# Performance work log

Measured on AMD Instinct MI355X. Metric: run time of the kernel, lower is better.

The kernel has to match this reference:

```python
import jax, jax.numpy as jnp
import numpy as np

D_MODEL = 1024
NUM_HEADS = 16
D_K = D_MODEL // NUM_HEADS
B, S = 2, 2048
LN_EPS = 1e-5


def setup_inputs() -> dict:
    key = jax.random.key(0)
    ks = jax.random.split(key, 11)
    sc = 1.0 / np.sqrt(D_MODEL)
    return {
        "x": jax.random.normal(ks[0], (B, S, D_MODEL), dtype=jnp.float32),
        "Wq": jax.random.normal(ks[1], (D_MODEL, D_MODEL), dtype=jnp.float32) * sc,
        "bq": jnp.zeros((D_MODEL,), dtype=jnp.float32),
        "Wk": jax.random.normal(ks[2], (D_MODEL, D_MODEL), dtype=jnp.float32) * sc,
        "bk": jnp.zeros((D_MODEL,), dtype=jnp.float32),
        "Wv": jax.random.normal(ks[3], (D_MODEL, D_MODEL), dtype=jnp.float32) * sc,
        "bv": jnp.zeros((D_MODEL,), dtype=jnp.float32),
        "Wo": jax.random.normal(ks[4], (D_MODEL, D_MODEL), dtype=jnp.float32) * sc,
        "bo": jnp.zeros((D_MODEL,), dtype=jnp.float32),
        "ln_gamma": jnp.ones((D_MODEL,), dtype=jnp.float32),
        "ln_beta": jnp.zeros((D_MODEL,), dtype=jnp.float32),
    }


def reference(x, Wq, bq, Wk, bk, Wv, bv, Wo, bo, ln_gamma, ln_beta):
    b, s, d = x.shape
    # QKV projections -> [B, H, S, D_K]
    def split_heads(y):
        return y.reshape(b, s, NUM_HEADS, D_K).transpose(0, 2, 1, 3)
    q = split_heads(x @ Wq + bq)
    k = split_heads(x @ Wk + bk)
    v = split_heads(x @ Wv + bv)
    # scores [B, H, S, S]; dropout is identity in eval mode
    scores = jnp.einsum("bhqd,bhkd->bhqk", q, k) / jnp.sqrt(jnp.float32(D_K))
    attn = jax.nn.softmax(scores, axis=-1)
    context = jnp.einsum("bhqk,bhkd->bhqd", attn, v)
    context = context.transpose(0, 2, 1, 3).reshape(b, s, d)
    out = context @ Wo + bo
    # residual + LayerNorm (eps=1e-5, torch default)
    h = x + out
    mu = jnp.mean(h, axis=-1, keepdims=True)
    var = jnp.var(h, axis=-1, keepdims=True)
    return (h - mu) / jnp.sqrt(var + LN_EPS) * ln_gamma + ln_beta
```

## Files before the change

### kernel.cpp

```cpp
#include <hip/hip_runtime.h>
#include <math.h>

#define D_MODEL 1024
#define NHEAD   16
#define DKK     64
#define BATCH   2
#define SEQ     2048
#define MROWS   (BATCH*SEQ)

typedef __attribute__((ext_vector_type(8)))  short bf16x8;
typedef __attribute__((ext_vector_type(4)))  short bf16x4;
typedef __attribute__((ext_vector_type(4)))  float f32x4;
typedef __attribute__((ext_vector_type(16))) float f32x16;

#define MFMA(a,b,c)   __builtin_amdgcn_mfma_f32_16x16x32_bf16((a),(b),(c),0,0,0)
#define MFMA32(a,b,c) __builtin_amdgcn_mfma_f32_32x32x16_bf16((a),(b),(c),0,0,0)

#define QSCALE 0.18033688f

#define SBAR() { __builtin_amdgcn_sched_barrier(0); \
                 __builtin_amdgcn_s_barrier();      \
                 __builtin_amdgcn_sched_barrier(0); }

#define CH  520
#define TIL (8*CH)

__device__ __forceinline__ short f2b(float f) {
    unsigned u = __float_as_uint(f);
    unsigned r = (u + 0x7FFFu + ((u >> 16) & 1u)) >> 16;
    return (short)r;
}

__device__ __forceinline__ float fexp2(float x) {
    float r; asm("v_exp_f32 %0, %1" : "=v"(r) : "v"(x)); return r;
}

__device__ __forceinline__ void gld_lds16(const void* g, void* l) {
    __builtin_amdgcn_global_load_lds(
        (const __attribute__((address_space(1))) void*)g,
        (__attribute__((address_space(3))) void*)l, 16, 0, 0);
}

__global__ __launch_bounds__(256)
void prep_weights(const float* __restrict__ Wq, const float* __restrict__ Wk,
                  const float* __restrict__ Wv, const float* __restrict__ Wo,
                  short* __restrict__ wt3, short* __restrict__ wot)
{
    const int z = blockIdx.z;
    const float* W = z==0 ? Wq : z==1 ? Wk : z==2 ? Wv : Wo;
    short* dst = (z < 3) ? (wt3 + (size_t)z*1024*1024) : wot;
    __shared__ float tile[32][33];
    const int tx = threadIdx.x & 31, ty = threadIdx.x >> 5;
    const int c0 = blockIdx.x*32, r0 = blockIdx.y*32;
    #pragma unroll
    for (int i = 0; i < 4; i++)
        tile[ty + i*8][tx] = W[(size_t)(r0 + ty + i*8)*1024 + c0 + tx];
    __syncthreads();
    #pragma unroll
    for (int i = 0; i < 4; i++)
        dst[(size_t)(c0 + ty + i*8)*1024 + r0 + tx] = f2b(tile[tx][ty + i*8]);
}

__global__ __launch_bounds__(256)
void convert_x(const float* __restrict__ x, short* __restrict__ xb)
{
    const int i = (blockIdx.x*256 + threadIdx.x) * 8;
    float4 a = *(const float4*)(x + i);
    float4 c = *(const float4*)(x + i + 4);
    bf16x8 v;
    v[0]=f2b(a.x); v[1]=f2b(a.y); v[2]=f2b(a.z); v[3]=f2b(a.w);
    v[4]=f2b(c.x); v[5]=f2b(c.y); v[6]=f2b(c.z); v[7]=f2b(c.w);
    *(bf16x8*)(xb + i) = v;
}

__global__ __launch_bounds__(512, 2)
void gemm_qkv(const short* __restrict__ A, const short* __restrict__ Bt,
              const float* __restrict__ bq, const float* __restrict__ bk,
              const float* __restrict__ bv,
              short* __restrict__ qb, short* __restrict__ kb, short* __restrict__ vtb)
{
    __shared__ short Ab[2*16384];
    __shared__ short Bb[2*12288];

    const int t = threadIdx.x;
    const int w = t >> 6, lane = t & 63;
    const int r = lane & 15, g4 = lane >> 4;
    const int wm = w >> 2, wn = w & 3;

    const int bid = blockIdx.x;
    const int xcd = bid & 7, idx = bid >> 3;
    const int mi  = (xcd >> 1) * 4 + (idx & 3);
    const int ni  = (xcd & 1) * 8 + (idx >> 2);
    const int m0 = mi * 256, n0 = ni * 192;

    const int srow = t >> 3;
    const int scol = ((t & 7) ^ (srow & 7)) * 8;

    f32x4 acc[8][3] = {};
    bf16x8 bfr[2][3];

#define QKV_STAGE(P, KT)                                                      \
    { const int kk = (KT) * 64 + scol;                                        \
      _Pragma("unroll")                                                       \
      for (int a = 0; a < 4; a++)                                             \
          gld_lds16(A + (size_t)(m0 + a*64 + srow)*1024 + kk,                 \
                    Ab + (P)*16384 + a*4096 + t*8);                           \
      _Pragma("unroll")                                                       \
      for (int p2 = 0; p2 < 3; p2++)                                          \
          gld_lds16(Bt + (size_t)(n0 + p2*64 + srow)*1024 + kk,               \
                    Bb + (P)*12288 + p2*4096 + t*8); }

#define QKV_PHASE(P, MH, KS, LOADB)                                           \
    { const short* Abase = Ab + (P)*16384 + wm*8192;                          \
      bf16x8 af[4];                                                           \
      _Pragma("unroll")                                                       \
      for (int i = 0; i < 4; i++)                                             \
          af[i] = *(const bf16x8*)&Abase[((MH)*64 + i*16 + r)*64 +            \
                                         (((KS)*4 + g4) ^ (r&7))*8];          \
      if (LOADB) {                                                            \
          const short* Bbase = Bb + (P)*12288;                                \
          _Pragma("unroll")                                                   \
          for (int j = 0; j < 3; j++)                                         \
              bfr[KS][j] = *(const bf16x8*)&Bbase[(wn*48 + j*16 + r)*64 +     \
                                                  (((KS)*4 + g4) ^ (r&7))*8]; \
      }                                                                       \
      SBAR();                                                                 \
      __builtin_amdgcn_s_setprio(1);                                          \
      _Pragma("unroll")                                                       \
      for (int i = 0; i < 4; i++)                                             \
          _Pragma("unroll")                                                   \
          for (int j = 0; j < 3; j++)                                         \
              acc[(MH)*4+i][j] = MFMA(af[i], bfr[KS][j], acc[(MH)*4+i][j]);   \
      __builtin_amdgcn_s_setprio(0);                                          \
      SBAR(); }

    QKV_STAGE(0, 0)
    QKV_STAGE(1, 1)
    asm volatile("s_waitcnt vmcnt(7)" ::: "memory");
    __builtin_amdgcn_s_barrier();
    __builtin_amdgcn_sched_barrier(0);

    int p = 0;
    #pragma unroll 1
    for (int kt = 0; kt < 16; kt++) {
        QKV_PHASE(p, 0, 0, 1)
        QKV_PHASE(p, 1, 0, 0)
        QKV_PHASE(p, 0, 1, 1)
        QKV_PHASE(p, 1, 1, 0)
        if (kt < 14) {
            QKV_STAGE(p, kt + 2)
            asm volatile("s_waitcnt vmcnt(7)" ::: "memory");
        } else {
            asm volatile("s_waitcnt vmcnt(0)" ::: "memory");
        }
        __builtin_amdgcn_s_barrier();
        __builtin_amdgcn_sched_barrier(0);
        p ^= 1;
    }
#undef QKV_STAGE
#undef QKV_PHASE

    #pragma unroll
    for (int n = 0; n < 3; n++) {
        const int colbase = n0 + wn*48 + n*16;
        const int proj    = colbase >> 10;
        const int within  = colbase & 1023;
        const int h       = within >> 6;
        const int d       = (within & 63) + r;
        const float* bias = (proj == 0) ? bq : (proj == 1) ? bk : bv;
        const float bval  = bias[within + r];
        #pragma unroll
        for (int m = 0; m < 8; m++) {
            const int growb = m0 + wm*128 + m*16 + g4*4;
            const int bidx  = growb >> 11;
            const int s     = growb & 2047;
            if (proj == 0) {
                #pragma unroll
                for (int i = 0; i < 4; i++)
                    qb[((size_t)(bidx*NHEAD + h)*SEQ + s + i)*DKK + d] =
                        f2b((acc[m][n][i] + bval) * QSCALE);
            } else if (proj == 1) {
                #pragma unroll
                for (int i = 0; i < 4; i++)
                    kb[((size_t)(bidx*NHEAD + h)*SEQ + s + i)*DKK + d] =
                        f2b(acc[m][n][i] + bval);
            } else {
                bf16x4 pk;
                #pragma unroll
                for (int i = 0; i < 4; i++) pk[i] = f2b(acc[m][n][i] + bval);
                *(bf16x4*)(vtb + ((size_t)(bidx*NHEAD + h)*DKK + d)*SEQ + s) = pk;
            }
        }
    }
}

__global__ __launch_bounds__(256)
void gemm_out(const short* __restrict__ A, const short* __restrict__ Bt,
              const float* __restrict__ bo, const float* __restrict__ resid,
              float* __restrict__ hb)
{
    __shared__ short As[2*128*32];
    __shared__ short Bs[2*64*32];
    const int t = threadIdx.x;
    const int w = t >> 6, lane = t & 63;
    const int r = lane & 15, g4 = lane >> 4;
    const int wr = w >> 1, wc = w & 1;

    const int bid = blockIdx.x;
    const int xcd = bid & 7, idx = bid >> 3;
    const int mi  = (xcd >> 1) * 8 + (idx & 7);
    const int ni  = (xcd & 1) * 8 + (idx >> 3);
    const int m0 = mi * 128, n0 = ni * 64;

    const int srow = lane >> 2, su = lane & 3;

    f32x4 acc[4][2] = {};

#define OUT_STAGE(BUF, K0)                                                     \
    { const int kk = (K0) & 1023;                                              \
      _Pragma("unroll")                                                        \
      for (int c = 0; c < 2; c++) {                                            \
          const int row = w*32 + c*16 + srow;                                  \
          gld_lds16(A + (size_t)(m0+row)*1024 + kk + 8*(su ^ ((row>>1)&3)),    \
                    As + (BUF)*4096 + w*1024 + c*512);                         \
      }                                                                        \
      { const int row = w*16 + srow;                                           \
        gld_lds16(Bt + (size_t)(n0+row)*1024 + kk + 8*(su ^ ((row>>1)&3)),     \
                  Bs + (BUF)*2048 + w*512); } }

    OUT_STAGE(0, 0)
    __syncthreads();

    int cur = 0;
    #pragma unroll 1
    for (int k0 = 0; k0 < 1024; k0 += 32) {
        OUT_STAGE(cur^1, k0 + 32)
        const short* Abase = As + cur*4096;
        const short* Bbase = Bs + cur*2048;
        bf16x8 af[4], bfr[2];
        #pragma unroll
        for (int m = 0; m < 4; m++) {
            const int row = wr*64 + m*16 + r;
            af[m] = *(const bf16x8*)&Abase[row*32 + (g4 ^ ((row>>1)&3))*8];
        }
        #pragma unroll
        for (int n = 0; n < 2; n++) {
            const int row = wc*32 + n*16 + r;
            bfr[n] = *(const bf16x8*)&Bbase[row*32 + (g4 ^ ((row>>1)&3))*8];
        }
        __builtin_amdgcn_s_setprio(1);
        #pragma unroll
        for (int m = 0; m < 4; m++)
            #pragma unroll
            for (int n = 0; n < 2; n++)
                acc[m][n] = MFMA(af[m], bfr[n], acc[m][n]);
        __builtin_amdgcn_s_setprio(0);
        __syncthreads();
        cur ^= 1;
    }
#undef OUT_STAGE

    #pragma unroll
    for (int n = 0; n < 2; n++) {
        const int col = n0 + wc*32 + n*16 + r;
        const float bval = bo[col];
        #pragma unroll
        for (int m = 0; m < 4; m++) {
            #pragma unroll
            for (int i = 0; i < 4; i++) {
                const int grow = m0 + wr*64 + m*16 + g4*4 + i;
                const size_t ofs = (size_t)grow*1024 + col;
                hb[ofs] = acc[m][n][i] + bval + resid[ofs];
            }
        }
    }
}

__global__ __launch_bounds__(256, 3)
void attn_mfma(const short* __restrict__ Q, const short* __restrict__ K,
               const short* __restrict__ VT, short* __restrict__ ctx)
{
    __shared__ short Ks[2*TIL];
    __shared__ short Vs[2*TIL];

    const int t = threadIdx.x;
    const int w = t >> 6, lane = t & 63;
    const int l31 = lane & 31, hi = lane >> 5;
    const int srow8 = lane >> 3, su = lane & 7;
    const int lane8 = lane * 8;
    const int swz8  = (su ^ srow8) * 8;

    const int bid     = blockIdx.x;
    const int logical = (bid & 7) * 64 + (bid >> 3);
    const int bh_lin  = logical >> 4;
    const int qt      = logical & 15;
    const int b = bh_lin >> 4, h = bh_lin & 15;
    const int q0 = qt * 128 + w * 32;

    const size_t bh = (size_t)b * NHEAD + h;
    const short* Qp = Q  + bh * SEQ * DKK;
    const short* Kp = K  + bh * SEQ * DKK;
    const short* Vp = VT + bh * DKK * SEQ;

    const short* kstage = Kp + (size_t)(w*8 + srow8) * DKK + swz8;
    const short* vstage = Vp + (size_t)(w*8 + srow8) * SEQ + swz8;

    bf16x8 qf[4];
    #pragma unroll
    for (int d0 = 0; d0 < 4; d0++)
        qf[d0] = *(const bf16x8*)(Qp + (size_t)(q0 + l31)*DKK + d0*16 + hi*8);

    int koff[8], voff[8];
    #pragma unroll
    for (int i = 0; i < 8; i++) {
        const int kchunk = (i>>2)*4 + (l31>>3);
        koff[i] = kchunk*CH + (l31&7)*64 + ((((i&3)*2 + hi) ^ (l31&7)) * 8);
        const int vchunk = (i&1)*4 + (l31>>3);
        voff[i] = vchunk*CH + (l31&7)*64 + ((((i>>1)*2 + hi) ^ (l31&7)) * 8);
    }

    f32x16 o0 = {}, o1 = {};
    float lrow = 0.f;

#define ATT_STAGE(KDST, VDST, J)                                               \
    { const size_t jj = (size_t)((J) & (SEQ-1));                               \
      const short* ksrc = kstage + jj*DKK;                                     \
      gld_lds16(ksrc,           (KDST) + w*CH + lane8);                        \
      gld_lds16(ksrc + 32*DKK,  (KDST) + (4+w)*CH + lane8);                    \
      const short* vsrc = vstage + jj;                                         \
      gld_lds16(vsrc,           (VDST) + w*CH + lane8);                        \
      gld_lds16(vsrc + 32*SEQ,  (VDST) + (4+w)*CH + lane8); }

    ATT_STAGE(Ks, Vs, 0)
    __syncthreads();

    int cur = 0;
    #pragma unroll 1
    for (int j0 = 0; j0 < SEQ; j0 += 64) {
        ATT_STAGE(Ks + (cur^1)*TIL, Vs + (cur^1)*TIL, j0 + 64)

        const short* Kb = Ks + cur*TIL;
        const short* Vb = Vs + cur*TIL;

        bf16x8 kf[8];
        #pragma unroll
        for (int i = 0; i < 8; i++) kf[i] = *(const bf16x8*)&Kb[koff[i]];
        f32x16 s0 = {}, s1 = {};
        __builtin_amdgcn_s_setprio(1);
        #pragma unroll
        for (int d0 = 0; d0 < 4; d0++) s0 = MFMA32(kf[d0],   qf[d0], s0);
        #pragma unroll
        for (int d0 = 0; d0 < 4; d0++) s1 = MFMA32(kf[4+d0], qf[d0], s1);
        __builtin_amdgcn_s_setprio(0);

        #pragma unroll
        for (int r = 0; r < 16; r++) s0[r] = fexp2(s0[r]);
        #pragma unroll
        for (int r = 0; r < 16; r++) s1[r] = fexp2(s1[r]);
        float ts[16];
        #pragma unroll
        for (int r = 0; r < 16; r++) ts[r] = s0[r] + s1[r];
        #pragma unroll
        for (int dd = 8; dd >= 1; dd >>= 1)
            #pragma unroll
            for (int r = 0; r < dd; r++) ts[r] += ts[r + dd];
        lrow += ts[0] + __shfl_xor(ts[0], 32);

        bf16x8 vf[8];
        #pragma unroll
        for (int i = 0; i < 8; i++) vf[i] = *(const bf16x8*)&Vb[voff[i]];

        #pragma unroll
        for (int ks = 0; ks < 4; ks++) {
            const int g = (ks & 1) * 8;
            float e0,e1,e2,e3,e4,e5,e6,e7;
            if (ks < 2) { e0=s0[g+0];e1=s0[g+1];e2=s0[g+2];e3=s0[g+3];
                          e4=s0[g+4];e5=s0[g+5];e6=s0[g+6];e7=s0[g+7]; }
            else        { e0=s1[g+0];e1=s1[g+1];e2=s1[g+2];e3=s1[g+3];
                          e4=s1[g+4];e5=s1[g+5];e6=s1[g+6];e7=s1[g+7]; }
            unsigned u0,u1,u2,u3;
            asm("v_cvt_pk_bf16_f32 %0, %1, %2" : "=v"(u0) : "v"(e0), "v"(e1));
            asm("v_cvt_pk_bf16_f32 %0, %1, %2" : "=v"(u1) : "v"(e2), "v"(e3));
            asm("v_cvt_pk_bf16_f32 %0, %1, %2" : "=v"(u2) : "v"(e4), "v"(e5));
            asm("v_cvt_pk_bf16_f32 %0, %1, %2" : "=v"(u3) : "v"(e6), "v"(e7));
            auto rA = __builtin_amdgcn_permlane32_swap(u0, u2, false, false);
            auto rB = __builtin_amdgcn_permlane32_swap(u1, u3, false, false);
            union { unsigned u[4]; bf16x8 v; } pa;
            pa.u[0] = rA[0]; pa.u[1] = rB[0]; pa.u[2] = rA[1]; pa.u[3] = rB[1];
            __builtin_amdgcn_s_setprio(1);
            o0 = MFMA32(pa.v, vf[ks*2+0], o0);
            o1 = MFMA32(pa.v, vf[ks*2+1], o1);
            __builtin_amdgcn_s_setprio(0);
        }

        __syncthreads();
        cur ^= 1;
    }

    const float li = 1.f / lrow;
    const int lb = __float_as_int(li);
    #pragma unroll
    for (int r = 0; r < 16; r++) {
        const int crow = (r&3) + 8*(r>>2) + 4*hi;
        const float lv = __int_as_float(__builtin_amdgcn_ds_bpermute(crow*4, lb));
        const size_t base = ((size_t)b*SEQ + q0 + crow)*D_MODEL + h*DKK + l31;
        ctx[base]      = f2b(o0[r] * lv);
        ctx[base + 32] = f2b(o1[r] * lv);
    }
#undef ATT_STAGE
}

__global__ __launch_bounds__(256)
void ln_kernel(const float* __restrict__ hbuf, const float* __restrict__ gamma,
               const float* __restrict__ beta, float* __restrict__ out)
{
    const int row = blockIdx.x;
    const int t = threadIdx.x;
    const float* hp = hbuf + (size_t)row * D_MODEL;
    float4 v = ((const float4*)hp)[t];
    float sum = v.x + v.y + v.z + v.w;
    float sq  = v.x*v.x + v.y*v.y + v.z*v.z + v.w*v.w;
    #pragma unroll
    for (int o = 1; o <= 32; o <<= 1) {
        sum += __shfl_xor(sum, o);
        sq  += __shfl_xor(sq, o);
    }
    __shared__ float s1[4], s2[4];
    if ((t & 63) == 0) { s1[t >> 6] = sum; s2[t >> 6] = sq; }
    __syncthreads();
    sum = s1[0] + s1[1] + s1[2] + s1[3];
    sq  = s2[0] + s2[1] + s2[2] + s2[3];
    const float mean = sum * (1.0f / D_MODEL);
    const float var  = sq * (1.0f / D_MODEL) - mean * mean;
    const float inv  = rsqrtf(var + 1e-5f);
    float4 g  = ((const float4*)gamma)[t];
    float4 be = ((const float4*)beta)[t];
    float4 rr;
    rr.x = (v.x - mean) * inv * g.x + be.x;
    rr.y = (v.y - mean) * inv * g.y + be.y;
    rr.z = (v.z - mean) * inv * g.z + be.z;
    rr.w = (v.w - mean) * inv * g.w + be.w;
    ((float4*)(out + (size_t)row * D_MODEL))[t] = rr;
}

extern "C" void kernel_launch(void* const* d_in, const int* in_sizes, int n_in,
                              void* d_out, int out_size, void* d_ws, size_t ws_size,
                              hipStream_t stream)
{
    const float* x  = (const float*)d_in[0];
    const float* Wq = (const float*)d_in[1];
    const float* bq = (const float*)d_in[2];
    const float* Wk = (const float*)d_in[3];
    const float* bk = (const float*)d_in[4];
    const float* Wv = (const float*)d_in[5];
    const float* bv = (const float*)d_in[6];
    const float* Wo = (const float*)d_in[7];
    const float* bo = (const float*)d_in[8];
    const float* g  = (const float*)d_in[9];
    const float* be = (const float*)d_in[10];

    short* xb  = (short*)d_ws;
    short* wt3 = xb  + (size_t)4096*1024;
    short* wot = wt3 + (size_t)3072*1024;
    short* qb  = wot + (size_t)1024*1024;
    short* kb  = qb  + (size_t)4096*1024;
    short* vtb = kb  + (size_t)4096*1024;
    short* cxb = vtb + (size_t)4096*1024;
    float* hb  = (float*)(cxb + (size_t)4096*1024);

    prep_weights<<<dim3(32,32,4), 256, 0, stream>>>(Wq, Wk, Wv, Wo, wt3, wot);
    convert_x  <<<2048, 256, 0, stream>>>(x, xb);
    gemm_qkv   <<<256, 512, 0, stream>>>(xb, wt3, bq, bk, bv, qb, kb, vtb);
    attn_mfma  <<<512, 256, 0, stream>>>(qb, kb, vtb, cxb);
    gemm_out   <<<512, 256, 0, stream>>>(cxb, wot, bo, x, hb);
    ln_kernel  <<<MROWS, 256, 0, stream>>>(hb, g, be, (float*)d_out);
}
```

Before: 124.7 us.

## Process two KV tiles per attention iteration with split accumulators

The attention loop now stages and processes 128 keys per iteration as two 64-key sub-tiles, with double-buffered LDS holding four tiles. The two halves use independent score and output accumulators, summed at the end. The aim is to halve the barrier count and give the scheduler more independent MFMA chains to overlap. In exchange LDS and register use roughly double, so launch bounds drop from 3 to 2 blocks per SIMD, lowering occupancy.

```diff
diff --git a/kernel.cpp b/kernel.cpp
--- a/kernel.cpp
+++ b/kernel.cpp
@@ -276,12 +276,12 @@
     }
 }
 
-__global__ __launch_bounds__(256, 3)
+__global__ __launch_bounds__(256, 2)
 void attn_mfma(const short* __restrict__ Q, const short* __restrict__ K,
                const short* __restrict__ VT, short* __restrict__ ctx)
 {
-    __shared__ short Ks[2*TIL];
-    __shared__ short Vs[2*TIL];
+    __shared__ short Ks[4*TIL];
+    __shared__ short Vs[4*TIL];
 
     const int t = threadIdx.x;
     const int w = t >> 6, lane = t & 63;
@@ -319,7 +319,7 @@
         voff[i] = vchunk*CH + (l31&7)*64 + ((((i>>1)*2 + hi) ^ (l31&7)) * 8);
     }
 
-    f32x16 o0 = {}, o1 = {};
+    f32x16 o0A = {}, o1A = {}, o0B = {}, o1B = {};
     float lrow = 0.f;
 
 #define ATT_STAGE(KDST, VDST, J)                                               \
@@ -331,67 +331,82 @@
       gld_lds16(vsrc,           (VDST) + w*CH + lane8);                        \
       gld_lds16(vsrc + 32*SEQ,  (VDST) + (4+w)*CH + lane8); }
 
-    ATT_STAGE(Ks, Vs, 0)
+#define QK_SUB(KB, S0, S1)                                                     \
+    { bf16x8 kf[8];                                                            \
+      _Pragma("unroll")                                                        \
+      for (int i = 0; i < 8; i++) kf[i] = *(const bf16x8*)&(KB)[koff[i]];      \
+      _Pragma("unroll")                                                        \
+      for (int d0 = 0; d0 < 4; d0++) S0 = MFMA32(kf[d0],   qf[d0], S0);        \
+      _Pragma("unroll")                                                        \
+      for (int d0 = 0; d0 < 4; d0++) S1 = MFMA32(kf[4+d0], qf[d0], S1); }
+
+#define PV_SUB(S0, S1, VB, O0, O1)                                             \
+    { bf16x8 vf[8];                                                            \
+      _Pragma("unroll")                                                        \
+      for (int i = 0; i < 8; i++) vf[i] = *(const bf16x8*)&(VB)[voff[i]];      \
+      _Pragma("unroll")                                                        \
+      for (int ks = 0; ks < 4; ks++) {                                         \
+        const int g = (ks & 1) * 8;                                            \
+        float e0,e1,e2,e3,e4,e5,e6,e7;                                         \
+        if (ks < 2) { e0=S0[g+0];e1=S0[g+1];e2=S0[g+2];e3=S0[g+3];             \
+                      e4=S0[g+4];e5=S0[g+5];e6=S0[g+6];e7=S0[g+7]; }           \
+        else        { e0=S1[g+0];e1=S1[g+1];e2=S1[g+2];e3=S1[g+3];             \
+                      e4=S1[g+4];e5=S1[g+5];e6=S1[g+6];e7=S1[g+7]; }           \
+        unsigned u0,u1,u2,u3;                                                  \
+        asm("v_cvt_pk_bf16_f32 %0, %1, %2" : "=v"(u0) : "v"(e0), "v"(e1));     \
+        asm("v_cvt_pk_bf16_f32 %0, %1, %2" : "=v"(u1) : "v"(e2), "v"(e3));     \
+        asm("v_cvt_pk_bf16_f32 %0, %1, %2" : "=v"(u2) : "v"(e4), "v"(e5));     \
+        asm("v_cvt_pk_bf16_f32 %0, %1, %2" : "=v"(u3) : "v"(e6), "v"(e7));     \
+        auto rA = __builtin_amdgcn_permlane32_swap(u0, u2, false, false);      \
+        auto rB = __builtin_amdgcn_permlane32_swap(u1, u3, false, false);      \
+        union { unsigned u[4]; bf16x8 v; } pa;                                 \
+        pa.u[0] = rA[0]; pa.u[1] = rB[0]; pa.u[2] = rA[1]; pa.u[3] = rB[1];    \
+        O0 = MFMA32(pa.v, vf[ks*2+0], O0);                                     \
+        O1 = MFMA32(pa.v, vf[ks*2+1], O1);                                     \
+      } }
+
+    ATT_STAGE(Ks,       Vs,       0)
+    ATT_STAGE(Ks + TIL, Vs + TIL, 64)
     __syncthreads();
 
     int cur = 0;
     #pragma unroll 1
-    for (int j0 = 0; j0 < SEQ; j0 += 64) {
-        ATT_STAGE(Ks + (cur^1)*TIL, Vs + (cur^1)*TIL, j0 + 64)
-
-        const short* Kb = Ks + cur*TIL;
-        const short* Vb = Vs + cur*TIL;
-
-        bf16x8 kf[8];
-        #pragma unroll
-        for (int i = 0; i < 8; i++) kf[i] = *(const bf16x8*)&Kb[koff[i]];
-        f32x16 s0 = {}, s1 = {};
-        __builtin_amdgcn_s_setprio(1);
-        #pragma unroll
-        for (int d0 = 0; d0 < 4; d0++) s0 = MFMA32(kf[d0],   qf[d0], s0);
-        #pragma unroll
-        for (int d0 = 0; d0 < 4; d0++) s1 = MFMA32(kf[4+d0], qf[d0], s1);
-        __builtin_amdgcn_s_setprio(0);
-
-        #pragma unroll
-        for (int r = 0; r < 16; r++) s0[r] = fexp2(s0[r]);
-        #pragma unroll
-        for (int r = 0; r < 16; r++) s1[r] = fexp2(s1[r]);
+    for (int j0 = 0; j0 < SEQ; j0 += 128) {
+        {
+            const int nb = (cur^1)*2*TIL;
+            ATT_STAGE(Ks + nb,       Vs + nb,       j0 + 128)
+            ATT_STAGE(Ks + nb + TIL, Vs + nb + TIL, j0 + 192)
+        }
+
+        const short* KbA = Ks + cur*2*TIL;
+        const short* VbA = Vs + cur*2*TIL;
+        const short* KbB = KbA + TIL;
+        const short* VbB = VbA + TIL;
+
+        f32x16 s0A = {}, s1A = {}, s0B = {}, s1B = {};
+        QK_SUB(KbA, s0A, s1A)
+        QK_SUB(KbB, s0B, s1B)
+
+        #pragma unroll
+        for (int r = 0; r < 16; r++) s0A[r] = fexp2(s0A[r]);
+        #pragma unroll
+        for (int r = 0; r < 16; r++) s1A[r] = fexp2(s1A[r]);
+        #pragma unroll
+        for (int r = 0; r < 16; r++) s0B[r] = fexp2(s0B[r]);
+        #pragma unroll
+        for (int r = 0; r < 16; r++) s1B[r] = fexp2(s1B[r]);
+
         float ts[16];
         #pragma unroll
-        for (int r = 0; r < 16; r++) ts[r] = s0[r] + s1[r];
+        for (int r = 0; r < 16; r++) ts[r] = (s0A[r] + s1A[r]) + (s0B[r] + s1B[r]);
         #pragma unroll
         for (int dd = 8; dd >= 1; dd >>= 1)
             #pragma unroll
             for (int r = 0; r < dd; r++) ts[r] += ts[r + dd];
         lrow += ts[0] + __shfl_xor(ts[0], 32);
 
-        bf16x8 vf[8];
-        #pragma unroll
-        for (int i = 0; i < 8; i++) vf[i] = *(const bf16x8*)&Vb[voff[i]];
-
-        #pragma unroll
-        for (int ks = 0; ks < 4; ks++) {
-            const int g = (ks & 1) * 8;
-            float e0,e1,e2,e3,e4,e5,e6,e7;
-            if (ks < 2) { e0=s0[g+0];e1=s0[g+1];e2=s0[g+2];e3=s0[g+3];
-                          e4=s0[g+4];e5=s0[g+5];e6=s0[g+6];e7=s0[g+7]; }
-            else        { e0=s1[g+0];e1=s1[g+1];e2=s1[g+2];e3=s1[g+3];
-                          e4=s1[g+4];e5=s1[g+5];e6=s1[g+6];e7=s1[g+7]; }
-            unsigned u0,u1,u2,u3;
-            asm("v_cvt_pk_bf16_f32 %0, %1, %2" : "=v"(u0) : "v"(e0), "v"(e1));
-            asm("v_cvt_pk_bf16_f32 %0, %1, %2" : "=v"(u1) : "v"(e2), "v"(e3));
-            asm("v_cvt_pk_bf16_f32 %0, %1, %2" : "=v"(u2) : "v"(e4), "v"(e5));
-            asm("v_cvt_pk_bf16_f32 %0, %1, %2" : "=v"(u3) : "v"(e6), "v"(e7));
-            auto rA = __builtin_amdgcn_permlane32_swap(u0, u2, false, false);
-            auto rB = __builtin_amdgcn_permlane32_swap(u1, u3, false, false);
-            union { unsigned u[4]; bf16x8 v; } pa;
-            pa.u[0] = rA[0]; pa.u[1] = rB[0]; pa.u[2] = rA[1]; pa.u[3] = rB[1];
-            __builtin_amdgcn_s_setprio(1);
-            o0 = MFMA32(pa.v, vf[ks*2+0], o0);
-            o1 = MFMA32(pa.v, vf[ks*2+1], o1);
-            __builtin_amdgcn_s_setprio(0);
-        }
+        PV_SUB(s0A, s1A, VbA, o0A, o1A)
+        PV_SUB(s0B, s1B, VbB, o0B, o1B)
 
         __syncthreads();
         cur ^= 1;
@@ -404,10 +419,12 @@
         const int crow = (r&3) + 8*(r>>2) + 4*hi;
         const float lv = __int_as_float(__builtin_amdgcn_ds_bpermute(crow*4, lb));
         const size_t base = ((size_t)b*SEQ + q0 + crow)*D_MODEL + h*DKK + l31;
-        ctx[base]      = f2b(o0[r] * lv);
-        ctx[base + 32] = f2b(o1[r] * lv);
+        ctx[base]      = f2b((o0A[r] + o0B[r]) * lv);
+        ctx[base + 32] = f2b((o1A[r] + o1B[r]) * lv);
     }
 #undef ATT_STAGE
+#undef QK_SUB
+#undef PV_SUB
 }
 
 __global__ __launch_bounds__(256)
```

After: 122.6 us. Within noise of the previous version (-1.6%).
